# Optimization experiments

Measured on AMD Instinct MI355X. Metric: run time of the kernel, lower is better.

Reference implementation:

```python
import jax, jax.numpy as jnp
import numpy as np

B, S, H = 4, 2048, 1024

def setup_inputs() -> dict:
    key = jax.random.key(0)
    ks = jax.random.split(key, 5)
    # xavier_uniform-ish scale (gain=0.1) for square weights: limit = 0.1*sqrt(6/(H+H))
    limit = 0.1 * np.sqrt(6.0 / (H + H))
    def w(k):
        return jax.random.uniform(k, (H, H), jnp.float32, -limit, limit)
    return {
        "x": jax.random.normal(ks[0], (B, S, H), jnp.float32),
        "W_i": w(ks[1]),
        "W_f": w(ks[2]),
        "W_g": w(ks[3]),
        "W_o": w(ks[4]),
    }

def _hgrn_forward(x, W_i, W_f, W_g, W_o):
    # Batched projections over all timesteps at once (nn.Linear: x @ W.T)
    f_sig = jax.nn.sigmoid(jnp.einsum('bsh,oh->bso', x, W_f))  # [B,S,H]
    i_raw = jnp.einsum('bsh,oh->bso', x, W_i)
    g = jnp.einsum('bsh,oh->bso', x, W_g)
    inp = i_raw * jax.nn.sigmoid(i_raw) * (1.0 - f_sig)        # SiLU(i)*(1-f)

    # Linear recurrence h_t = f_t * h_{t-1} + inp_t via scan over time
    f_t = jnp.moveaxis(f_sig, 1, 0)  # [S,B,H]
    i_t = jnp.moveaxis(inp, 1, 0)
    h0 = jnp.zeros((x.shape[0], x.shape[2]), x.dtype)

    def step(h, fi):
        f, i = fi
        h = f * h + i
        return h, h

    _, h_all = jax.lax.scan(step, h0, (f_t, i_t))  # [S,B,H]
    h_all = jnp.moveaxis(h_all, 0, 1)              # [B,S,H]

    return jnp.einsum('bsh,oh->bso', g * h_all, W_o)

def reference(x, W_i, W_f, W_g, W_o):
    return _hgrn_forward(x, W_i, W_f, W_g, W_o)
```

## Files before the change

kernel.cpp:

```cpp
#include <hip/hip_runtime.h>

#define Bb 4
#define Ss 2048
#define Hh 1024
#define Mm (Bb * Ss)
#define NC 64
#define CL 32

typedef _Float16 f16;
typedef _Float16 f16x2 __attribute__((ext_vector_type(2)));
typedef _Float16 f16x4 __attribute__((ext_vector_type(4)));
typedef _Float16 f16x8 __attribute__((ext_vector_type(8)));
typedef float    f32x4 __attribute__((ext_vector_type(4)));

__device__ __forceinline__ float sigf(float z) { return 1.0f / (1.0f + __expf(-z)); }

__device__ __forceinline__ void gl2lds16(const f16* g, f16* l) {
    __builtin_amdgcn_global_load_lds(
        (const __attribute__((address_space(1))) void*)g,
        (__attribute__((address_space(3))) void*)l,
        16, 0, 0);
}

__global__ __launch_bounds__(256) void conv_all(
    const float* __restrict__ x,
    const float* __restrict__ W0, const float* __restrict__ W1,
    const float* __restrict__ W2, const float* __restrict__ W3,
    f16* __restrict__ xh, f16* __restrict__ wh)
{
    const int i  = blockIdx.x * 256 + threadIdx.x;
    const int nx = (Mm * Hh) / 4;
    if (i < nx) {
        const float4 v = ((const float4*)x)[i];
        const float vv[4] = {v.x, v.y, v.z, v.w};
        f16x4 h4;
        #pragma unroll
        for (int q = 0; q < 4; ++q) h4[q] = (f16)vv[q];
        ((f16x4*)xh)[i] = h4;
    } else {
        const int j = i - nx;
        const int which = j >> 18;
        const int r = j & 262143;
        const float* src = (which == 0) ? W0 : (which == 1) ? W1 : (which == 2) ? W2 : W3;
        const float4 v = ((const float4*)src)[r];
        const float vv[4] = {v.x, v.y, v.z, v.w};
        f16x4 h4;
        #pragma unroll
        for (int q = 0; q < 4; ++q) h4[q] = (f16)vv[q];
        ((f16x4*)wh)[j] = h4;
    }
}


#define RD_A(j) { ah[j] = *(const f16x8*)(cb +         (wr4 + (j)) * 512 + lo); }
#define RD_B(j) { bv[j] = *(const f16x8*)(cb + 4096 + (wc4 + (j)) * 512 + lo); }

#define MM(mi, ni) acc[mi][ni] = __builtin_amdgcn_mfma_f32_16x16x32_f16(ah[mi], bv[ni], acc[mi][ni], 0, 0, 0);

#define KSTEP1(cbP, sbP, kn, STG) do { \
    const f16* cb = (cbP); \
    if (STG) { \
        gl2lds16(gp[0] + (kn), (sbP) + lb[0] + lo); \
        gl2lds16(gp[1] + (kn), (sbP) + lb[1] + lo); \
        gl2lds16(gp[2] + (kn), (sbP) + lb[2] + lo); \
    } \
    RD_A(0) RD_B(0) RD_A(1) RD_B(1) \
    RD_A(2) RD_B(2) RD_A(3) RD_B(3) \
    __builtin_amdgcn_s_setprio(1); \
    MM(0,0) MM(0,1) MM(0,2) MM(0,3) \
    MM(1,0) MM(1,1) MM(1,2) MM(1,3) \
    MM(2,0) MM(2,1) MM(2,2) MM(2,3) \
    MM(3,0) MM(3,1) MM(3,2) MM(3,3) \
    __builtin_amdgcn_s_setprio(0); \
} while (0)

__global__ __launch_bounds__(512, 4) void gemm_split(
    const f16* __restrict__ Ap, const f16* __restrict__ Bp,
    float* __restrict__ C0, int ld0, float* __restrict__ C1, int ld1, int nsplit)
{
    __shared__ __align__(16) f16 lds[3][12288];

    const int tid  = threadIdx.x;
    const int lane = tid & 63;
    const int wave = tid >> 6;
    const int wr4  = (wave >> 2) * 4;
    const int wc4  = (wave & 3) * 4;
    const int lm   = lane & 15;
    const int kq   = lane >> 4;
    const int lo   = lane * 8;

    const int nwg = gridDim.x * gridDim.y;
    const int bid = blockIdx.y * gridDim.x + blockIdx.x;
    const int swz = (bid & 7) * (nwg >> 3) + (bid >> 3);
    const int m0  = (swz / gridDim.x) * 128;
    const int n0  = (swz % gridDim.x) * 256;

    const f16* gp[3];
    int lb[3];
    #pragma unroll
    for (int i = 0; i < 3; ++i) {
        const int blk = wave * 3 + i;
        lb[i] = blk * 512;
        const f16* base; int row;
        if (blk < 8) { base = Ap; row = m0 + blk * 16; }
        else         { base = Bp; row = n0 + (blk - 8) * 16; }
        gp[i] = base + (size_t)(row + lm) * Hh + kq * 8;
    }

    f32x4 acc[4][4] = {};
    f16x8 ah[4], bv[4];

    f16* b0 = &lds[0][0];
    f16* b1 = &lds[1][0];
    f16* b2 = &lds[2][0];

    #pragma unroll
    for (int i = 0; i < 3; ++i) gl2lds16(gp[i],      b0 + lb[i] + lo);
    #pragma unroll
    for (int i = 0; i < 3; ++i) gl2lds16(gp[i] + 32, b1 + lb[i] + lo);
    asm volatile("s_waitcnt vmcnt(3)" ::: "memory");
    __builtin_amdgcn_s_barrier();

    #pragma unroll 1
    for (int t = 0; t < 30; ++t) {
        KSTEP1(b0, b2, (t + 2) * 32, true);
        asm volatile("s_waitcnt vmcnt(3)" ::: "memory");
        __builtin_amdgcn_s_barrier();
        f16* tmp = b0; b0 = b1; b1 = b2; b2 = tmp;
    }
    KSTEP1(b0, b2, 0, false);
    asm volatile("s_waitcnt vmcnt(0)" ::: "memory");
    __builtin_amdgcn_s_barrier();
    KSTEP1(b1, b2, 0, false);

    #pragma unroll
    for (int mi = 0; mi < 4; ++mi)
        #pragma unroll
        for (int ni = 0; ni < 4; ++ni) {
            const int n = n0 + (wc4 >> 2) * 64 + ni * 16 + lm;
            const bool sec = (n >= nsplit);
            float* Cp  = sec ? C1 : C0;
            const int ld = sec ? ld1 : ld0;
            const int nn = sec ? n - nsplit : n;
            #pragma unroll
            for (int r = 0; r < 4; ++r) {
                const int m = m0 + (wr4 >> 2) * 64 + mi * 16 + kq * 4 + r;
                Cp[(size_t)m * ld + nn] = acc[mi][ni][r];
            }
        }
}

__global__ __launch_bounds__(256) void scan1(
    const float* __restrict__ zif, float4* __restrict__ csum)
{
    const int g  = blockIdx.x * 256 + threadIdx.x;
    const int c  = g >> 11;
    const int p  = g & 2047;
    const int b  = p >> 9, h = (p & 511) * 2;
    const size_t base = (size_t)b * Ss * 2048 + h;
    const int s0 = c * CL;
    float P0 = 1.0f, L0 = 0.0f, P1 = 1.0f, L1 = 0.0f;
    for (int j = 0; j < CL; j += 4) {
        float2 zi[4], zf[4];
        #pragma unroll
        for (int q = 0; q < 4; ++q) {
            const size_t off = base + (size_t)(s0 + j + q) * 2048;
            zi[q] = *(const float2*)(zif + off);
            zf[q] = *(const float2*)(zif + off + 1024);
        }
        #pragma unroll
        for (int q = 0; q < 4; ++q) {
            const float f0  = sigf(zf[q].x);
            const float ip0 = zi[q].x * sigf(zi[q].x) * (1.0f - f0);
            L0 = fmaf(f0, L0, ip0); P0 *= f0;
            const float f1  = sigf(zf[q].y);
            const float ip1 = zi[q].y * sigf(zi[q].y) * (1.0f - f1);
            L1 = fmaf(f1, L1, ip1); P1 *= f1;
        }
    }
    csum[(size_t)p * NC + c] = make_float4(P0, L0, P1, L1);
}

__global__ __launch_bounds__(256) void scan2(
    const float* __restrict__ zif, const float* __restrict__ zg,
    const float4* __restrict__ csum, f16* __restrict__ ghh)
{
    const int g  = blockIdx.x * 256 + threadIdx.x;
    const int c  = g >> 11;
    const int p  = g & 2047;
    const int b  = p >> 9, h = (p & 511) * 2;
    const size_t base  = (size_t)b * Ss * 2048 + h;
    const size_t baseg = (size_t)b * Ss * 1024 + h;
    float h0 = 0.0f, h1 = 0.0f;
    for (int cp = 0; cp < c; ++cp) {
        const float4 pl = csum[(size_t)p * NC + cp];
        h0 = fmaf(pl.x, h0, pl.y);
        h1 = fmaf(pl.z, h1, pl.w);
    }
    const int s0 = c * CL;
    for (int j = 0; j < CL; j += 4) {
        float2 zi[4], zf[4], gv[4];
        #pragma unroll
        for (int q = 0; q < 4; ++q) {
            const size_t off = base + (size_t)(s0 + j + q) * 2048;
            zi[q] = *(const float2*)(zif + off);
            zf[q] = *(const float2*)(zif + off + 1024);
            gv[q] = *(const float2*)(zg + baseg + (size_t)(s0 + j + q) * 1024);
        }
        #pragma unroll
        for (int q = 0; q < 4; ++q) {
            const float f0  = sigf(zf[q].x);
            const float ip0 = zi[q].x * sigf(zi[q].x) * (1.0f - f0);
            h0 = fmaf(f0, h0, ip0);
            const float f1  = sigf(zf[q].y);
            const float ip1 = zi[q].y * sigf(zi[q].y) * (1.0f - f1);
            h1 = fmaf(f1, h1, ip1);
            f16x2 vh;
            vh[0] = (f16)(gv[q].x * h0);
            vh[1] = (f16)(gv[q].y * h1);
            *(f16x2*)(ghh + baseg + (size_t)(s0 + j + q) * 1024) = vh;
        }
    }
}

__global__ __launch_bounds__(256) void proj_kernel(
    const float* __restrict__ x,  const float* __restrict__ Wi,
    const float* __restrict__ Wf, const float* __restrict__ Wg,
    float* __restrict__ f_out, float* __restrict__ inp_out, float* __restrict__ g_out)
{
    __shared__ __align__(16) float As [16][68];
    __shared__ __align__(16) float Bis[16][68];
    __shared__ __align__(16) float Bfs[16][68];
    __shared__ __align__(16) float Bgs[16][68];
    const int tid = threadIdx.x;
    const int tx = tid & 15, ty = tid >> 4;
    const int m0 = blockIdx.x * 64, n0 = blockIdx.y * 64;
    const int lr = tid >> 2, lk = (tid & 3) << 2;
    float acc_i[4][4] = {}, acc_f[4][4] = {}, acc_g[4][4] = {};
    const float* pA = x  + (size_t)(m0 + lr) * Hh + lk;
    const float* pI = Wi + (size_t)(n0 + lr) * Hh + lk;
    const float* pF = Wf + (size_t)(n0 + lr) * Hh + lk;
    const float* pG = Wg + (size_t)(n0 + lr) * Hh + lk;
    for (int k0 = 0; k0 < Hh; k0 += 16) {
        const float4 av = *(const float4*)(pA + k0);
        const float4 iv = *(const float4*)(pI + k0);
        const float4 fv = *(const float4*)(pF + k0);
        const float4 gv = *(const float4*)(pG + k0);
        __syncthreads();
        As [lk+0][lr] = av.x; As [lk+1][lr] = av.y; As [lk+2][lr] = av.z; As [lk+3][lr] = av.w;
        Bis[lk+0][lr] = iv.x; Bis[lk+1][lr] = iv.y; Bis[lk+2][lr] = iv.z; Bis[lk+3][lr] = iv.w;
        Bfs[lk+0][lr] = fv.x; Bfs[lk+1][lr] = fv.y; Bfs[lk+2][lr] = fv.z; Bfs[lk+3][lr] = fv.w;
        Bgs[lk+0][lr] = gv.x; Bgs[lk+1][lr] = gv.y; Bgs[lk+2][lr] = gv.z; Bgs[lk+3][lr] = gv.w;
        __syncthreads();
        #pragma unroll
        for (int kk = 0; kk < 16; ++kk) {
            const float4 a  = *(const float4*)&As [kk][ty << 2];
            const float4 bi = *(const float4*)&Bis[kk][tx << 2];
            const float4 bf = *(const float4*)&Bfs[kk][tx << 2];
            const float4 bg = *(const float4*)&Bgs[kk][tx << 2];
            const float aa[4]  = {a.x,a.y,a.z,a.w};
            const float bbi[4] = {bi.x,bi.y,bi.z,bi.w};
            const float bbf[4] = {bf.x,bf.y,bf.z,bf.w};
            const float bbg[4] = {bg.x,bg.y,bg.z,bg.w};
            #pragma unroll
            for (int i = 0; i < 4; ++i)
                #pragma unroll
                for (int j = 0; j < 4; ++j) {
                    acc_i[i][j] = fmaf(aa[i], bbi[j], acc_i[i][j]);
                    acc_f[i][j] = fmaf(aa[i], bbf[j], acc_f[i][j]);
                    acc_g[i][j] = fmaf(aa[i], bbg[j], acc_g[i][j]);
                }
        }
    }
    #pragma unroll
    for (int i = 0; i < 4; ++i) {
        const size_t row = (size_t)(m0 + (ty << 2) + i) * Hh + n0 + (tx << 2);
        float4 vf, vp, vg;
        float* qf = (float*)&vf; float* qp = (float*)&vp; float* qg = (float*)&vg;
        #pragma unroll
        for (int j = 0; j < 4; ++j) {
            const float ff = sigf(acc_f[i][j]);
            const float zi = acc_i[i][j];
            qf[j] = ff; qp[j] = zi * sigf(zi) * (1.0f - ff); qg[j] = acc_g[i][j];
        }
        *(float4*)(f_out + row) = vf;
        *(float4*)(inp_out + row) = vp;
        *(float4*)(g_out + row) = vg;
    }
}

__global__ __launch_bounds__(256) void recur_kernel(
    const float* f_buf, const float* __restrict__ inp_buf,
    const float* __restrict__ g_buf, float* gh_out)
{
    const int t = blockIdx.x * 256 + threadIdx.x;
    const int b = t >> 10, h = t & 1023;
    const size_t base = (size_t)b * Ss * Hh + h;
    float hh = 0.0f;
    for (int s0 = 0; s0 < Ss; s0 += 8) {
        float fr[8], ir[8], gr[8], o[8];
        #pragma unroll
        for (int j = 0; j < 8; ++j) {
            const size_t off = base + (size_t)(s0 + j) * Hh;
            fr[j] = f_buf[off]; ir[j] = inp_buf[off]; gr[j] = g_buf[off];
        }
        #pragma unroll
        for (int j = 0; j < 8; ++j) { hh = fmaf(fr[j], hh, ir[j]); o[j] = gr[j] * hh; }
        #pragma unroll
        for (int j = 0; j < 8; ++j) gh_out[base + (size_t)(s0 + j) * Hh] = o[j];
    }
}

__global__ __launch_bounds__(256) void out_kernel(
    const float* __restrict__ A, const float* __restrict__ Wo, float* __restrict__ out)
{
    __shared__ __align__(16) float As[16][68];
    __shared__ __align__(16) float Bs[16][68];
    const int tid = threadIdx.x;
    const int tx = tid & 15, ty = tid >> 4;
    const int m0 = blockIdx.x * 64, n0 = blockIdx.y * 64;
    const int lr = tid >> 2, lk = (tid & 3) << 2;
    float acc[4][4] = {};
    const float* pA = A  + (size_t)(m0 + lr) * Hh + lk;
    const float* pB = Wo + (size_t)(n0 + lr) * Hh + lk;
    for (int k0 = 0; k0 < Hh; k0 += 16) {
        const float4 av = *(const float4*)(pA + k0);
        const float4 bv = *(const float4*)(pB + k0);
        __syncthreads();
        As[lk+0][lr] = av.x; As[lk+1][lr] = av.y; As[lk+2][lr] = av.z; As[lk+3][lr] = av.w;
        Bs[lk+0][lr] = bv.x; Bs[lk+1][lr] = bv.y; Bs[lk+2][lr] = bv.z; Bs[lk+3][lr] = bv.w;
        __syncthreads();
        #pragma unroll
        for (int kk = 0; kk < 16; ++kk) {
            const float4 a = *(const float4*)&As[kk][ty << 2];
            const float4 b = *(const float4*)&Bs[kk][tx << 2];
            const float aa[4] = {a.x,a.y,a.z,a.w};
            const float bb[4] = {b.x,b.y,b.z,b.w};
            #pragma unroll
            for (int i = 0; i < 4; ++i)
                #pragma unroll
                for (int j = 0; j < 4; ++j)
                    acc[i][j] = fmaf(aa[i], bb[j], acc[i][j]);
        }
    }
    #pragma unroll
    for (int i = 0; i < 4; ++i) {
        const size_t row = (size_t)(m0 + (ty << 2) + i) * Hh + n0 + (tx << 2);
        float4 v;
        ((float*)&v)[0]=acc[i][0]; ((float*)&v)[1]=acc[i][1];
        ((float*)&v)[2]=acc[i][2]; ((float*)&v)[3]=acc[i][3];
        *(float4*)(out + row) = v;
    }
}

extern "C" void kernel_launch(void* const* d_in, const int* in_sizes, int n_in,
                              void* d_out, int out_size, void* d_ws, size_t ws_size,
                              hipStream_t stream) {
    const float* x  = (const float*)d_in[0];
    const float* Wi = (const float*)d_in[1];
    const float* Wf = (const float*)d_in[2];
    const float* Wg = (const float*)d_in[3];
    const float* Wo = (const float*)d_in[4];
    float* out = (float*)d_out;

    const size_t MH = (size_t)Mm * Hh;
    const size_t HH = (size_t)Hh * Hh;

    size_t need = MH*2 + HH*4*2 + MH*2*4 + MH*2 + (size_t)2048*NC*16;

    if (ws_size >= need) {
        char* p = (char*)d_ws;
        f16* xh      = (f16*)p;    p += MH*2;
        f16* Wh      = (f16*)p;    p += HH*4*2;
        float* zif   = (float*)p;  p += MH*2*4;
        f16* ghh     = (f16*)p;    p += MH*2;
        float4* csum = (float4*)p;

        const int nconv = (int)(MH/4 + HH);
        conv_all<<<nconv/256, 256, 0, stream>>>(x, Wi, Wf, Wg, Wo, xh, Wh);

        gemm_split<<<dim3(12, 64), 512, 0, stream>>>(
            xh, Wh, zif, 2048, out, 1024, 2048);

        scan1<<<512, 256, 0, stream>>>(zif, csum);
        scan2<<<512, 256, 0, stream>>>(zif, out, csum, ghh);

        gemm_split<<<dim3(4, 64), 512, 0, stream>>>(
            ghh, Wh + 3*HH, out, 1024, out, 1024, 1 << 30);
    } else {
        float* f_buf   = (float*)d_ws;
        float* inp_buf = f_buf + MH;
        dim3 grid(Mm / 64, Hh / 64);
        proj_kernel<<<grid, 256, 0, stream>>>(x, Wi, Wf, Wg, f_buf, inp_buf, out);
        recur_kernel<<<16, 256, 0, stream>>>(f_buf, inp_buf, out, f_buf);
        out_kernel<<<grid, 256, 0, stream>>>(f_buf, Wo, out);
    }
}
```

Baseline: 244.3 us.

## Replace LDS-staged GEMM pipeline with direct global-to-register double-buffered loads

The GEMM no longer stages A/B tiles through a triple-buffered LDS pipeline fed by global_load_lds. Each wave now loads its own A and B fragments straight from global memory into registers, double-buffered across 32-wide K steps, which removes the LDS traffic and barriers. Occupancy bound drops from 4 to 2 blocks per CU to fit the extra registers. Fragments shared between waves are now fetched redundantly from global/L2 (each A row is read by 4 waves, each B row by 2), raising cache bandwidth demand, and the loads are 16-byte strided row accesses that are less coalesced.

```diff
diff --git a/kernel.cpp b/kernel.cpp
--- a/kernel.cpp
+++ b/kernel.cpp
@@ -14,13 +14,6 @@
 typedef float    f32x4 __attribute__((ext_vector_type(4)));
 
 __device__ __forceinline__ float sigf(float z) { return 1.0f / (1.0f + __expf(-z)); }
-
-__device__ __forceinline__ void gl2lds16(const f16* g, f16* l) {
-    __builtin_amdgcn_global_load_lds(
-        (const __attribute__((address_space(1))) void*)g,
-        (__attribute__((address_space(3))) void*)l,
-        16, 0, 0);
-}
 
 __global__ __launch_bounds__(256) void conv_all(
     const float* __restrict__ x,
@@ -52,42 +45,47 @@
 }
 
 
-#define RD_A(j) { ah[j] = *(const f16x8*)(cb +         (wr4 + (j)) * 512 + lo); }
-#define RD_B(j) { bv[j] = *(const f16x8*)(cb + 4096 + (wc4 + (j)) * 512 + lo); }
-
-#define MM(mi, ni) acc[mi][ni] = __builtin_amdgcn_mfma_f32_16x16x32_f16(ah[mi], bv[ni], acc[mi][ni], 0, 0, 0);
-
-#define KSTEP1(cbP, sbP, kn, STG) do { \
-    const f16* cb = (cbP); \
-    if (STG) { \
-        gl2lds16(gp[0] + (kn), (sbP) + lb[0] + lo); \
-        gl2lds16(gp[1] + (kn), (sbP) + lb[1] + lo); \
-        gl2lds16(gp[2] + (kn), (sbP) + lb[2] + lo); \
-    } \
-    RD_A(0) RD_B(0) RD_A(1) RD_B(1) \
-    RD_A(2) RD_B(2) RD_A(3) RD_B(3) \
+#define LOADF(aR, bR, kk) { \
+    aR[0] = *(const f16x8*)(pa +                 (kk)); \
+    aR[1] = *(const f16x8*)(pa + 16 * Hh +       (kk)); \
+    aR[2] = *(const f16x8*)(pa + 32 * Hh +       (kk)); \
+    aR[3] = *(const f16x8*)(pa + 48 * Hh +       (kk)); \
+    bR[0] = *(const f16x8*)(pb +                 (kk)); \
+    bR[1] = *(const f16x8*)(pb + 16 * Hh +       (kk)); \
+    bR[2] = *(const f16x8*)(pb + 32 * Hh +       (kk)); \
+    bR[3] = *(const f16x8*)(pb + 48 * Hh +       (kk)); }
+
+#define MMALL(aR, bR) { \
     __builtin_amdgcn_s_setprio(1); \
-    MM(0,0) MM(0,1) MM(0,2) MM(0,3) \
-    MM(1,0) MM(1,1) MM(1,2) MM(1,3) \
-    MM(2,0) MM(2,1) MM(2,2) MM(2,3) \
-    MM(3,0) MM(3,1) MM(3,2) MM(3,3) \
-    __builtin_amdgcn_s_setprio(0); \
-} while (0)
-
-__global__ __launch_bounds__(512, 4) void gemm_split(
+    acc[0][0] = __builtin_amdgcn_mfma_f32_16x16x32_f16(aR[0], bR[0], acc[0][0], 0, 0, 0); \
+    acc[0][1] = __builtin_amdgcn_mfma_f32_16x16x32_f16(aR[0], bR[1], acc[0][1], 0, 0, 0); \
+    acc[0][2] = __builtin_amdgcn_mfma_f32_16x16x32_f16(aR[0], bR[2], acc[0][2], 0, 0, 0); \
+    acc[0][3] = __builtin_amdgcn_mfma_f32_16x16x32_f16(aR[0], bR[3], acc[0][3], 0, 0, 0); \
+    acc[1][0] = __builtin_amdgcn_mfma_f32_16x16x32_f16(aR[1], bR[0], acc[1][0], 0, 0, 0); \
+    acc[1][1] = __builtin_amdgcn_mfma_f32_16x16x32_f16(aR[1], bR[1], acc[1][1], 0, 0, 0); \
+    acc[1][2] = __builtin_amdgcn_mfma_f32_16x16x32_f16(aR[1], bR[2], acc[1][2], 0, 0, 0); \
+    acc[1][3] = __builtin_amdgcn_mfma_f32_16x16x32_f16(aR[1], bR[3], acc[1][3], 0, 0, 0); \
+    acc[2][0] = __builtin_amdgcn_mfma_f32_16x16x32_f16(aR[2], bR[0], acc[2][0], 0, 0, 0); \
+    acc[2][1] = __builtin_amdgcn_mfma_f32_16x16x32_f16(aR[2], bR[1], acc[2][1], 0, 0, 0); \
+    acc[2][2] = __builtin_amdgcn_mfma_f32_16x16x32_f16(aR[2], bR[2], acc[2][2], 0, 0, 0); \
+    acc[2][3] = __builtin_amdgcn_mfma_f32_16x16x32_f16(aR[2], bR[3], acc[2][3], 0, 0, 0); \
+    acc[3][0] = __builtin_amdgcn_mfma_f32_16x16x32_f16(aR[3], bR[0], acc[3][0], 0, 0, 0); \
+    acc[3][1] = __builtin_amdgcn_mfma_f32_16x16x32_f16(aR[3], bR[1], acc[3][1], 0, 0, 0); \
+    acc[3][2] = __builtin_amdgcn_mfma_f32_16x16x32_f16(aR[3], bR[2], acc[3][2], 0, 0, 0); \
+    acc[3][3] = __builtin_amdgcn_mfma_f32_16x16x32_f16(aR[3], bR[3], acc[3][3], 0, 0, 0); \
+    __builtin_amdgcn_s_setprio(0); }
+
+__global__ __launch_bounds__(512, 2) void gemm_direct(
     const f16* __restrict__ Ap, const f16* __restrict__ Bp,
     float* __restrict__ C0, int ld0, float* __restrict__ C1, int ld1, int nsplit)
 {
-    __shared__ __align__(16) f16 lds[3][12288];
-
     const int tid  = threadIdx.x;
     const int lane = tid & 63;
     const int wave = tid >> 6;
-    const int wr4  = (wave >> 2) * 4;
-    const int wc4  = (wave & 3) * 4;
+    const int wr   = wave >> 2;
+    const int wc   = wave & 3;
     const int lm   = lane & 15;
     const int kq   = lane >> 4;
-    const int lo   = lane * 8;
 
     const int nwg = gridDim.x * gridDim.y;
     const int bid = blockIdx.y * gridDim.x + blockIdx.x;
@@ -95,56 +93,36 @@
     const int m0  = (swz / gridDim.x) * 128;
     const int n0  = (swz % gridDim.x) * 256;
 
-    const f16* gp[3];
-    int lb[3];
-    #pragma unroll
-    for (int i = 0; i < 3; ++i) {
-        const int blk = wave * 3 + i;
-        lb[i] = blk * 512;
-        const f16* base; int row;
-        if (blk < 8) { base = Ap; row = m0 + blk * 16; }
-        else         { base = Bp; row = n0 + (blk - 8) * 16; }
-        gp[i] = base + (size_t)(row + lm) * Hh + kq * 8;
-    }
+    const f16* pa = Ap + (size_t)(m0 + wr * 64 + lm) * Hh + kq * 8;
+    const f16* pb = Bp + (size_t)(n0 + wc * 64 + lm) * Hh + kq * 8;
 
     f32x4 acc[4][4] = {};
-    f16x8 ah[4], bv[4];
-
-    f16* b0 = &lds[0][0];
-    f16* b1 = &lds[1][0];
-    f16* b2 = &lds[2][0];
-
-    #pragma unroll
-    for (int i = 0; i < 3; ++i) gl2lds16(gp[i],      b0 + lb[i] + lo);
-    #pragma unroll
-    for (int i = 0; i < 3; ++i) gl2lds16(gp[i] + 32, b1 + lb[i] + lo);
-    asm volatile("s_waitcnt vmcnt(3)" ::: "memory");
-    __builtin_amdgcn_s_barrier();
-
+    f16x8 a0[4], b0[4], a1[4], b1[4];
+
+    LOADF(a0, b0, 0);
     #pragma unroll 1
-    for (int t = 0; t < 30; ++t) {
-        KSTEP1(b0, b2, (t + 2) * 32, true);
-        asm volatile("s_waitcnt vmcnt(3)" ::: "memory");
-        __builtin_amdgcn_s_barrier();
-        f16* tmp = b0; b0 = b1; b1 = b2; b2 = tmp;
-    }
-    KSTEP1(b0, b2, 0, false);
-    asm volatile("s_waitcnt vmcnt(0)" ::: "memory");
-    __builtin_amdgcn_s_barrier();
-    KSTEP1(b1, b2, 0, false);
+    for (int k = 0; k < Hh - 64; k += 64) {
+        LOADF(a1, b1, k + 32);
+        MMALL(a0, b0);
+        LOADF(a0, b0, k + 64);
+        MMALL(a1, b1);
+    }
+    LOADF(a1, b1, Hh - 32);
+    MMALL(a0, b0);
+    MMALL(a1, b1);
 
     #pragma unroll
     for (int mi = 0; mi < 4; ++mi)
         #pragma unroll
         for (int ni = 0; ni < 4; ++ni) {
-            const int n = n0 + (wc4 >> 2) * 64 + ni * 16 + lm;
+            const int n = n0 + wc * 64 + ni * 16 + lm;
             const bool sec = (n >= nsplit);
             float* Cp  = sec ? C1 : C0;
             const int ld = sec ? ld1 : ld0;
             const int nn = sec ? n - nsplit : n;
             #pragma unroll
             for (int r = 0; r < 4; ++r) {
-                const int m = m0 + (wr4 >> 2) * 64 + mi * 16 + kq * 4 + r;
+                const int m = m0 + wr * 64 + mi * 16 + kq * 4 + r;
                 Cp[(size_t)m * ld + nn] = acc[mi][ni][r];
             }
         }
@@ -379,13 +357,13 @@
         const int nconv = (int)(MH/4 + HH);
         conv_all<<<nconv/256, 256, 0, stream>>>(x, Wi, Wf, Wg, Wo, xh, Wh);
 
-        gemm_split<<<dim3(12, 64), 512, 0, stream>>>(
+        gemm_direct<<<dim3(12, 64), 512, 0, stream>>>(
             xh, Wh, zif, 2048, out, 1024, 2048);
 
         scan1<<<512, 256, 0, stream>>>(zif, csum);
         scan2<<<512, 256, 0, stream>>>(zif, out, csum, ghh);
 
-        gemm_split<<<dim3(4, 64), 512, 0, stream>>>(
+        gemm_direct<<<dim3(4, 64), 512, 0, stream>>>(
             ghh, Wh + 3*HH, out, 1024, out, 1024, 1 << 30);
     } else {
         float* f_buf   = (float*)d_ws;
```

New measurement: 375.4 us. +53.7%, slower.
